# Optimization experiments

Hardware: AMD Instinct MI355X
Metric: run time of the kernel (lower is better)

## Reference

```python
import jax, jax.numpy as jnp
import numpy as np

B, S, H = 4, 4096, 1024
NUM_LEVELS, DECAY = 3, 0.8
D0, D1 = 512, 204  # int(1024*0.5), int(512*0.5*0.8)


def _xavier(key, shape):
    fan_in, fan_out = shape
    return jax.random.normal(key, shape, dtype=jnp.float32) * np.sqrt(2.0 / (fan_in + fan_out))


def setup_inputs() -> dict:
    key = jax.random.key(0)
    ks = jax.random.split(key, 8)
    return {
        "keys": jax.random.normal(ks[0], (B, S, H), dtype=jnp.float32),
        "values": jax.random.normal(ks[1], (B, S, H), dtype=jnp.float32),
        "importance": jax.random.uniform(ks[2], (B, S), dtype=jnp.float32),
        # encoder layers (stored as [in, out]; torch Linear applies x @ W.T + b)
        "We0": _xavier(ks[3], (H, D0)), "be0": jnp.zeros((D0,), jnp.float32),
        "We1": _xavier(ks[4], (D0, D1)), "be1": jnp.zeros((D1,), jnp.float32),
        # decoder layers
        "Wd0": _xavier(ks[5], (D0, H)), "bd0": jnp.zeros((H,), jnp.float32),
        "Wd1": _xavier(ks[6], (D1, D0)), "bd1": jnp.zeros((D0,), jnp.float32),
    }


def _level_sizes(n):
    sizes, remaining = [], n
    for i in range(NUM_LEVELS):
        if i == NUM_LEVELS - 1:
            sizes.append(remaining)
        else:
            sz = int(remaining * (1 - DECAY) * DECAY ** i)
            sizes.append(sz)
            remaining -= sz
    return sizes


def reference(keys, values, importance, We0, be0, We1, be1, Wd0, bd0, Wd1, bd1):
    n = B * S
    fk = keys.reshape(n, H)
    fv = values.reshape(n, H)
    sorted_idx = jnp.argsort(-importance.reshape(-1))  # descending importance
    sizes = _level_sizes(n)

    def chain(x, level):
        # encode 0..level-1 with ReLU, then decode level-1..0 with ReLU
        if level >= 1:
            x = jax.nn.relu(x @ We0 + be0)
        if level >= 2:
            x = jax.nn.relu(x @ We1 + be1)
            x = jax.nn.relu(x @ Wd1 + bd1)
        if level >= 1:
            x = jax.nn.relu(x @ Wd0 + bd0)
        return x

    ck = jnp.zeros_like(fk)
    cv = jnp.zeros_like(fv)
    start = 0
    for level, size in enumerate(sizes):
        if size <= 0:
            continue
        idx = jax.lax.dynamic_slice(sorted_idx, (start,), (size,))
        ck = ck.at[idx].set(chain(fk[idx], level))
        cv = cv.at[idx].set(chain(fv[idx], level))
        start += size
    return ck.reshape(B, S, H), cv.reshape(B, S, H)
```

## Files before the change

kernel.cpp:

```cpp
#include <hip/hip_runtime.h>

typedef __attribute__((ext_vector_type(8))) short short8;
typedef __attribute__((ext_vector_type(4))) float f32x4;

#define N_TOK   16384
#define HDIM    1024
#define OUT_OFF 16777216
#define M1ROWS  26216
#define M2ROWS  22022
#define L2ROW0  4194

__device__ __forceinline__ unsigned short f2bf(float f) {
  unsigned int u = __float_as_uint(f);
  u += 0x7FFFu + ((u >> 16) & 1u);
  return (unsigned short)(u >> 16);
}

__device__ __forceinline__ void rowmap(int r, int& is_v, int& rank) {
  if (r < 2097)       { is_v = 0; rank = 3276 + r; }
  else if (r < 4194)  { is_v = 1; rank = 1179 + r; }
  else if (r < 15205) { is_v = 0; rank = 1179 + r; }
  else                { is_v = 1; rank = r - 9832; }
}

__global__ __launch_bounds__(256) void rank_count(const float* __restrict__ imp,
                                                  int* __restrict__ counts) {
  __shared__ float sj[2048];
  const int i = blockIdx.x * 256 + threadIdx.x;
  const int jbase = blockIdx.y * 2048;
  const float vi = imp[i];
  for (int s = threadIdx.x; s < 2048; s += 256) sj[s] = imp[jbase + s];
  __syncthreads();
  int cnt = 0;
  #pragma unroll 8
  for (int s = 0; s < 2048; ++s) {
    float vj = sj[s];
    bool gt = vj > vi;
    bool eq = (vj == vi) && ((jbase + s) < i);
    cnt += (gt || eq) ? 1 : 0;
  }
  atomicAdd(&counts[i], cnt);
}

__global__ __launch_bounds__(256) void scatter_order(const int* __restrict__ counts,
                                                     int* __restrict__ order) {
  int i = blockIdx.x * 256 + threadIdx.x;
  order[counts[i]] = i;
}

__global__ __launch_bounds__(256) void prep_fused(
    unsigned short* __restrict__ We0T, const float* __restrict__ We0,
    unsigned short* __restrict__ We1T, const float* __restrict__ We1,
    unsigned short* __restrict__ Wd1T, const float* __restrict__ Wd1,
    unsigned short* __restrict__ Wd0T, const float* __restrict__ Wd0,
    unsigned short* __restrict__ X,
    const float* __restrict__ keys, const float* __restrict__ values,
    const int* __restrict__ order, float* __restrict__ out) {
  int b = blockIdx.x;
  if (b < 5120) {
    unsigned short* dst; const float* src; int Kd, Nsrc, Ksrc, idx;
    if (b < 2048)      { dst = We0T; src = We0; Kd = 1024; Nsrc = 512;  Ksrc = 1024; idx = b * 256 + threadIdx.x; }
    else if (b < 2560) { dst = We1T; src = We1; Kd = 512;  Nsrc = 204;  Ksrc = 512;  idx = (b - 2048) * 256 + threadIdx.x; }
    else if (b < 3072) { dst = Wd1T; src = Wd1; Kd = 256;  Nsrc = 512;  Ksrc = 204;  idx = (b - 2560) * 256 + threadIdx.x; }
    else               { dst = Wd0T; src = Wd0; Kd = 512;  Nsrc = 1024; Ksrc = 512;  idx = (b - 3072) * 256 + threadIdx.x; }
    int n = idx / Kd, k = idx % Kd;
    float v = (n < Nsrc && k < Ksrc) ? src[k * Nsrc + n] : 0.f;
    dst[idx] = f2bf(v);
  } else if (b < 5120 + 6554) {
    int r = (b - 5120) * 4 + (threadIdx.x >> 6);
    int lane = threadIdx.x & 63;
    int is_v, rank; rowmap(r, is_v, rank);
    int token = order[rank];
    const float* src = (is_v ? values : keys) + (size_t)token * HDIM + lane * 16;
    float4 f0 = *reinterpret_cast<const float4*>(src);
    float4 f1 = *reinterpret_cast<const float4*>(src + 4);
    float4 f2 = *reinterpret_cast<const float4*>(src + 8);
    float4 f3 = *reinterpret_cast<const float4*>(src + 12);
    unsigned short* dst = X + (size_t)r * HDIM + lane * 16;
    ushort4 h;
    h.x = f2bf(f0.x); h.y = f2bf(f0.y); h.z = f2bf(f0.z); h.w = f2bf(f0.w);
    *reinterpret_cast<ushort4*>(dst) = h;
    h.x = f2bf(f1.x); h.y = f2bf(f1.y); h.z = f2bf(f1.z); h.w = f2bf(f1.w);
    *reinterpret_cast<ushort4*>(dst + 4) = h;
    h.x = f2bf(f2.x); h.y = f2bf(f2.y); h.z = f2bf(f2.z); h.w = f2bf(f2.w);
    *reinterpret_cast<ushort4*>(dst + 8) = h;
    h.x = f2bf(f3.x); h.y = f2bf(f3.y); h.z = f2bf(f3.z); h.w = f2bf(f3.w);
    *reinterpret_cast<ushort4*>(dst + 12) = h;
  } else {
    int idx = (b - (5120 + 6554)) * 4 + (threadIdx.x >> 6);
    int lane = threadIdx.x & 63;
    int is_v = idx & 1, rank = idx >> 1;
    int token = order[rank];
    const float* src = (is_v ? values : keys) + (size_t)token * HDIM + lane * 16;
    float* dst = out + (is_v ? OUT_OFF : 0) + (size_t)token * HDIM + lane * 16;
    float4 f0 = *reinterpret_cast<const float4*>(src);
    float4 f1 = *reinterpret_cast<const float4*>(src + 4);
    float4 f2 = *reinterpret_cast<const float4*>(src + 8);
    float4 f3 = *reinterpret_cast<const float4*>(src + 12);
    *reinterpret_cast<float4*>(dst)      = f0;
    *reinterpret_cast<float4*>(dst + 4)  = f1;
    *reinterpret_cast<float4*>(dst + 8)  = f2;
    *reinterpret_cast<float4*>(dst + 12) = f3;
  }
}

#define GLDS16(g, l) __builtin_amdgcn_global_load_lds( \
    (const __attribute__((address_space(1))) void*)(g), \
    (__attribute__((address_space(3))) void*)(l), 16, 0, 0)

template<int MODE, int K>
__global__ __launch_bounds__(256, 4) void g128(
    const unsigned short* __restrict__ A, int M,
    const unsigned short* __restrict__ Bt, int N,
    const float* __restrict__ bias, int Nbias,
    unsigned short* __restrict__ Cbf, int ldc,
    float* __restrict__ outf, const int* __restrict__ order,
    int NP, int NC) {
  constexpr int NH = K / 32;
  __shared__ __align__(16) unsigned short S[3][8192];

  const int bid = blockIdx.x;
  const int r8 = bid & 7, rest = bid >> 3;
  const int c8 = rest % NC, q8 = rest / NC;
  const int p8 = q8 * 8 + r8;
  if (p8 >= NP) return;
  const int row0 = p8 * 128, col0 = c8 * 128;

  const int tid = threadIdx.x;
  const int wave = tid >> 6, lane = tid & 63;
  const int wm = wave >> 1, wn = wave & 1;
  const int fr = lane & 15, lch = lane >> 4;

  const int lrow = lane >> 2;
  const int sswz = (((lane & 3) ^ ((lane >> 3) & 3)) << 3);
  const unsigned short* gp[4];
  int ldso[4];
  #pragma unroll
  for (int j = 0; j < 4; ++j) {
    const int g = wave * 4 + j;
    const bool isA = g < 8;
    int rr = isA ? (row0 + g * 16 + lrow) : (col0 + (g - 8) * 16 + lrow);
    const int lim = isA ? M : N;
    if (rr >= lim) rr = 0;
    gp[j] = (isA ? A : Bt) + (size_t)rr * K + sswz;
    ldso[j] = g * 512;
  }

  const int qoff = ((lch ^ ((fr >> 1) & 3)) << 3);
  const int abase = (wm * 64 + fr) * 32 + qoff;
  const int bbase = 4096 + (wn * 64 + fr) * 32 + qoff;

  f32x4 acc[4][4] = {};

  #pragma unroll
  for (int j = 0; j < 4; ++j) GLDS16(gp[j], S[0] + ldso[j]);
  #pragma unroll
  for (int j = 0; j < 4; ++j) GLDS16(gp[j] + 32, S[1] + ldso[j]);

  int cur = 0;
  #pragma unroll 1
  for (int t = 0; t < NH; ++t) {
    if (t + 1 < NH) asm volatile("s_waitcnt vmcnt(4)" ::: "memory");
    else            asm volatile("s_waitcnt vmcnt(0)" ::: "memory");
    __builtin_amdgcn_s_barrier();
    __builtin_amdgcn_sched_barrier(0);
    const unsigned short* sl = S[cur];
    short8 a[4], b[4];
    #pragma unroll
    for (int m = 0; m < 4; ++m)
      a[m] = *reinterpret_cast<const short8*>(sl + abase + m * 512);
    #pragma unroll
    for (int n = 0; n < 4; ++n)
      b[n] = *reinterpret_cast<const short8*>(sl + bbase + n * 512);
    if (t + 2 < NH) {
      const int kc = (t + 2) * 32;
      int nb = cur + 2; if (nb >= 3) nb -= 3;
      #pragma unroll
      for (int j = 0; j < 4; ++j) GLDS16(gp[j] + kc, S[nb] + ldso[j]);
    }
    #pragma unroll
    for (int m = 0; m < 4; ++m)
      #pragma unroll
      for (int n = 0; n < 4; ++n)
        acc[m][n] = __builtin_amdgcn_mfma_f32_16x16x32_bf16(a[m], b[n], acc[m][n], 0, 0, 0);
    cur = (cur == 2) ? 0 : cur + 1;
  }

  const int orow = lch * 4;
  if (MODE == 0) {
    #pragma unroll
    for (int m = 0; m < 4; ++m)
      #pragma unroll
      for (int n = 0; n < 4; ++n)
        #pragma unroll
        for (int j = 0; j < 4; ++j) {
          int r = row0 + wm * 64 + m * 16 + orow + j;
          int c = col0 + wn * 64 + n * 16 + fr;
          if (r < M && c < N) {
            float v = acc[m][n][j] + (c < Nbias ? bias[c] : 0.f);
            Cbf[(size_t)r * ldc + c] = f2bf(fmaxf(v, 0.f));
          }
        }
  } else {
    float* Cl = (float*)S;
    #pragma unroll 1
    for (int p = 0; p < 2; ++p) {
      __builtin_amdgcn_s_barrier();
      if (wm == p) {
        #pragma unroll
        for (int m = 0; m < 4; ++m)
          #pragma unroll
          for (int n = 0; n < 4; ++n)
            #pragma unroll
            for (int j = 0; j < 4; ++j) {
              int rr = m * 16 + orow + j;
              int cc = wn * 64 + n * 16 + fr;
              float v = acc[m][n][j] + bias[col0 + cc];
              Cl[rr * 132 + cc] = fmaxf(v, 0.f);
            }
      }
      __builtin_amdgcn_s_barrier();
      #pragma unroll
      for (int u = 0; u < 8; ++u) {
        int unit = tid + u * 256;
        int rr = unit >> 5, ch = unit & 31;
        int r = row0 + p * 64 + rr;
        if (r < M) {
          int iv, rk; rowmap(r, iv, rk);
          int token = order[rk];
          f32x4 v = *reinterpret_cast<const f32x4*>(Cl + rr * 132 + ch * 4);
          *reinterpret_cast<f32x4*>(outf + (size_t)(iv ? OUT_OFF : 0) +
                                    (size_t)token * HDIM + col0 + ch * 4) = v;
        }
      }
    }
  }
}

static inline int swzg(int NP, int NC) { return 8 * NC * ((NP + 7) / 8); }

extern "C" void kernel_launch(void* const* d_in, const int* in_sizes, int n_in,
                              void* d_out, int out_size, void* d_ws, size_t ws_size,
                              hipStream_t stream) {
  const float* keys   = (const float*)d_in[0];
  const float* values = (const float*)d_in[1];
  const float* imp    = (const float*)d_in[2];
  const float* We0    = (const float*)d_in[3];
  const float* be0    = (const float*)d_in[4];
  const float* We1    = (const float*)d_in[5];
  const float* be1    = (const float*)d_in[6];
  const float* Wd0    = (const float*)d_in[7];
  const float* bd0    = (const float*)d_in[8];
  const float* Wd1    = (const float*)d_in[9];
  const float* bd1    = (const float*)d_in[10];

  char* ws = (char*)d_ws;
  int* counts           = (int*)(ws);
  int* order            = (int*)(ws + 65536);
  unsigned short* We0T  = (unsigned short*)(ws + 131072);
  unsigned short* We1T  = (unsigned short*)(ws + 1179648);
  unsigned short* Wd1T  = (unsigned short*)(ws + 1441792);
  unsigned short* Wd0T  = (unsigned short*)(ws + 1703936);
  unsigned short* Y     = (unsigned short*)(ws + 2752512);
  unsigned short* Z     = (unsigned short*)(ws + 29597696);
  unsigned short* X     = (unsigned short*)(ws + 40872960);
  float* outf = (float*)d_out;

  hipMemsetAsync(counts, 0, 65536, stream);
  rank_count<<<dim3(64, 8), 256, 0, stream>>>(imp, counts);
  scatter_order<<<64, 256, 0, stream>>>(counts, order);

  prep_fused<<<5120 + 6554 + 1638, 256, 0, stream>>>(
      We0T, We0, We1T, We1, Wd1T, Wd1, Wd0T, Wd0, X, keys, values, order, outf);

  g128<0, 1024><<<swzg(205, 4), 256, 0, stream>>>(
      X, M1ROWS, We0T, 512, be0, 512, Y, 512, nullptr, nullptr, 205, 4);

  g128<0, 512><<<swzg(173, 2), 256, 0, stream>>>(
      Y + (size_t)L2ROW0 * 512, M2ROWS, We1T, 256, be1, 204, Z, 256,
      nullptr, nullptr, 173, 2);

  g128<0, 256><<<swzg(173, 4), 256, 0, stream>>>(
      Z, M2ROWS, Wd1T, 512, bd1, 512, Y + (size_t)L2ROW0 * 512, 512,
      nullptr, nullptr, 173, 4);

  g128<1, 512><<<swzg(205, 8), 256, 0, stream>>>(
      Y, M1ROWS, Wd0T, 1024, bd0, 1024, nullptr, 0, outf, order, 205, 8);
}
```

Measured before the change: 275.9 us.

## Double-buffer GEMM LDS, raise occupancy, and tile weight transpose through LDS

The GEMM main loop drops from a triple-buffered LDS ring to a double buffer, adding a second barrier after the fragment reads so the next prefetch can safely overwrite the same slot. This shrinks shared memory enough to ask for 5 workgroups per CU, and the MFMA block runs at raised wave priority. The weight transpose/bf16 conversion moves into its own kernel that uses 64x64 LDS tiles so both global reads and writes are coalesced. The extra barrier per K step shortens the prefetch distance and could expose memory latency. The epilogue LDS stride changes from 132 to 128, which may add bank conflicts.

```diff
diff --git a/kernel.cpp b/kernel.cpp
--- a/kernel.cpp
+++ b/kernel.cpp
@@ -48,27 +48,43 @@
   order[counts[i]] = i;
 }
 
-__global__ __launch_bounds__(256) void prep_fused(
+__global__ __launch_bounds__(256) void wtrans4(
     unsigned short* __restrict__ We0T, const float* __restrict__ We0,
     unsigned short* __restrict__ We1T, const float* __restrict__ We1,
     unsigned short* __restrict__ Wd1T, const float* __restrict__ Wd1,
-    unsigned short* __restrict__ Wd0T, const float* __restrict__ Wd0,
+    unsigned short* __restrict__ Wd0T, const float* __restrict__ Wd0) {
+  __shared__ float Tl[64][65];
+  int b = blockIdx.x;
+  const float* src; unsigned short* dst; int Ks, Ns, Kd, tk, tn;
+  if (b < 128)      { src = We0; dst = We0T; Ks = 1024; Ns = 512;  Kd = 1024; tk = b >> 3;          tn = b & 7; }
+  else if (b < 256) { src = Wd0; dst = Wd0T; Ks = 512;  Ns = 1024; Kd = 512;  tk = (b - 128) >> 4;  tn = (b - 128) & 15; }
+  else if (b < 288) { src = We1; dst = We1T; Ks = 512;  Ns = 204;  Kd = 512;  tk = (b - 256) >> 2;  tn = (b - 256) & 3; }
+  else              { src = Wd1; dst = Wd1T; Ks = 204;  Ns = 512;  Kd = 256;  tk = (b - 288) >> 3;  tn = (b - 288) & 7; }
+  const int k0 = tk * 64, n0 = tn * 64;
+  const int t = threadIdx.x;
+  const int cl = t & 63, rw = t >> 6;
+  #pragma unroll
+  for (int i = 0; i < 16; ++i) {
+    int kl = i * 4 + rw;
+    int k = k0 + kl, n = n0 + cl;
+    Tl[kl][cl] = (k < Ks && n < Ns) ? src[(size_t)k * Ns + n] : 0.f;
+  }
+  __syncthreads();
+  #pragma unroll
+  for (int i = 0; i < 16; ++i) {
+    int nl = i * 4 + rw;
+    dst[(size_t)(n0 + nl) * Kd + (k0 + cl)] = f2bf(Tl[cl][nl]);
+  }
+}
+
+__global__ __launch_bounds__(256) void gathercopy(
     unsigned short* __restrict__ X,
     const float* __restrict__ keys, const float* __restrict__ values,
     const int* __restrict__ order, float* __restrict__ out) {
   int b = blockIdx.x;
-  if (b < 5120) {
-    unsigned short* dst; const float* src; int Kd, Nsrc, Ksrc, idx;
-    if (b < 2048)      { dst = We0T; src = We0; Kd = 1024; Nsrc = 512;  Ksrc = 1024; idx = b * 256 + threadIdx.x; }
-    else if (b < 2560) { dst = We1T; src = We1; Kd = 512;  Nsrc = 204;  Ksrc = 512;  idx = (b - 2048) * 256 + threadIdx.x; }
-    else if (b < 3072) { dst = Wd1T; src = Wd1; Kd = 256;  Nsrc = 512;  Ksrc = 204;  idx = (b - 2560) * 256 + threadIdx.x; }
-    else               { dst = Wd0T; src = Wd0; Kd = 512;  Nsrc = 1024; Ksrc = 512;  idx = (b - 3072) * 256 + threadIdx.x; }
-    int n = idx / Kd, k = idx % Kd;
-    float v = (n < Nsrc && k < Ksrc) ? src[k * Nsrc + n] : 0.f;
-    dst[idx] = f2bf(v);
-  } else if (b < 5120 + 6554) {
-    int r = (b - 5120) * 4 + (threadIdx.x >> 6);
-    int lane = threadIdx.x & 63;
+  int lane = threadIdx.x & 63;
+  if (b < 6554) {
+    int r = b * 4 + (threadIdx.x >> 6);
     int is_v, rank; rowmap(r, is_v, rank);
     int token = order[rank];
     const float* src = (is_v ? values : keys) + (size_t)token * HDIM + lane * 16;
@@ -87,8 +103,7 @@
     h.x = f2bf(f3.x); h.y = f2bf(f3.y); h.z = f2bf(f3.z); h.w = f2bf(f3.w);
     *reinterpret_cast<ushort4*>(dst + 12) = h;
   } else {
-    int idx = (b - (5120 + 6554)) * 4 + (threadIdx.x >> 6);
-    int lane = threadIdx.x & 63;
+    int idx = (b - 6554) * 4 + (threadIdx.x >> 6);
     int is_v = idx & 1, rank = idx >> 1;
     int token = order[rank];
     const float* src = (is_v ? values : keys) + (size_t)token * HDIM + lane * 16;
@@ -109,7 +124,7 @@
     (__attribute__((address_space(3))) void*)(l), 16, 0, 0)
 
 template<int MODE, int K>
-__global__ __launch_bounds__(256, 4) void g128(
+__global__ __launch_bounds__(256, 5) void g128(
     const unsigned short* __restrict__ A, int M,
     const unsigned short* __restrict__ Bt, int N,
     const float* __restrict__ bias, int Nbias,
@@ -117,7 +132,7 @@
     float* __restrict__ outf, const int* __restrict__ order,
     int NP, int NC) {
   constexpr int NH = K / 32;
-  __shared__ __align__(16) unsigned short S[3][8192];
+  __shared__ __align__(16) unsigned short S[2][8192];
 
   const int bid = blockIdx.x;
   const int r8 = bid & 7, rest = bid >> 3;
@@ -157,14 +172,14 @@
   #pragma unroll
   for (int j = 0; j < 4; ++j) GLDS16(gp[j] + 32, S[1] + ldso[j]);
 
-  int cur = 0;
   #pragma unroll 1
   for (int t = 0; t < NH; ++t) {
+    const int s = t & 1;
     if (t + 1 < NH) asm volatile("s_waitcnt vmcnt(4)" ::: "memory");
     else            asm volatile("s_waitcnt vmcnt(0)" ::: "memory");
     __builtin_amdgcn_s_barrier();
     __builtin_amdgcn_sched_barrier(0);
-    const unsigned short* sl = S[cur];
+    const unsigned short* sl = S[s];
     short8 a[4], b[4];
     #pragma unroll
     for (int m = 0; m < 4; ++m)
@@ -172,18 +187,21 @@
     #pragma unroll
     for (int n = 0; n < 4; ++n)
       b[n] = *reinterpret_cast<const short8*>(sl + bbase + n * 512);
+    asm volatile("s_waitcnt lgkmcnt(0)" ::: "memory");
+    __builtin_amdgcn_sched_barrier(0);
+    __builtin_amdgcn_s_barrier();
     if (t + 2 < NH) {
       const int kc = (t + 2) * 32;
-      int nb = cur + 2; if (nb >= 3) nb -= 3;
       #pragma unroll
-      for (int j = 0; j < 4; ++j) GLDS16(gp[j] + kc, S[nb] + ldso[j]);
+      for (int j = 0; j < 4; ++j) GLDS16(gp[j] + kc, S[s] + ldso[j]);
     }
+    __builtin_amdgcn_s_setprio(1);
     #pragma unroll
     for (int m = 0; m < 4; ++m)
       #pragma unroll
       for (int n = 0; n < 4; ++n)
         acc[m][n] = __builtin_amdgcn_mfma_f32_16x16x32_bf16(a[m], b[n], acc[m][n], 0, 0, 0);
-    cur = (cur == 2) ? 0 : cur + 1;
+    __builtin_amdgcn_s_setprio(0);
   }
 
   const int orow = lch * 4;
@@ -216,7 +234,7 @@
               int rr = m * 16 + orow + j;
               int cc = wn * 64 + n * 16 + fr;
               float v = acc[m][n][j] + bias[col0 + cc];
-              Cl[rr * 132 + cc] = fmaxf(v, 0.f);
+              Cl[rr * 128 + cc] = fmaxf(v, 0.f);
             }
       }
       __builtin_amdgcn_s_barrier();
@@ -228,7 +246,7 @@
         if (r < M) {
           int iv, rk; rowmap(r, iv, rk);
           int token = order[rk];
-          f32x4 v = *reinterpret_cast<const f32x4*>(Cl + rr * 132 + ch * 4);
+          f32x4 v = *reinterpret_cast<const f32x4*>(Cl + rr * 128 + ch * 4);
           *reinterpret_cast<f32x4*>(outf + (size_t)(iv ? OUT_OFF : 0) +
                                     (size_t)token * HDIM + col0 + ch * 4) = v;
         }
@@ -270,8 +288,8 @@
   rank_count<<<dim3(64, 8), 256, 0, stream>>>(imp, counts);
   scatter_order<<<64, 256, 0, stream>>>(counts, order);
 
-  prep_fused<<<5120 + 6554 + 1638, 256, 0, stream>>>(
-      We0T, We0, We1T, We1, Wd1T, Wd1, Wd0T, Wd0, X, keys, values, order, outf);
+  wtrans4<<<320, 256, 0, stream>>>(We0T, We0, We1T, We1, Wd1T, Wd1, Wd0T, Wd0);
+  gathercopy<<<6554 + 1638, 256, 0, stream>>>(X, keys, values, order, outf);
 
   g128<0, 1024><<<swzg(205, 4), 256, 0, stream>>>(
       X, M1ROWS, We0T, 512, be0, 512, Y, 512, nullptr, nullptr, 205, 4);
```

New measurement: 476.3 us. 72.6% more time.
